# Optimization experiments

Measured on AMD Instinct MI355X. Metric: run time of the kernel, lower is better.

The kernel has to match this reference:

```python
import jax, jax.numpy as jnp
import numpy as np

N, C, W_DIM, H_DIM = 2, 256, 64, 64
HEADS = 4
DH = C // HEADS  # per-head dim for Q,K,V projections
EPS = 1e-5


def _layernorm(x, w, b):
    mu = jnp.mean(x, axis=-1, keepdims=True)
    var = jnp.var(x, axis=-1, keepdims=True)
    return (x - mu) * jax.lax.rsqrt(var + EPS) * w + b


def setup_inputs() -> dict:
    key = jax.random.key(0)
    ks = jax.random.split(key, 12)
    s = 1.0 / np.sqrt(C)
    return {
        "x": jax.random.normal(ks[0], (N, C, W_DIM, H_DIM), dtype=jnp.float32),
        "ln1_w": jnp.ones((C,), jnp.float32),
        "ln1_b": jnp.zeros((C,), jnp.float32),
        # per-head projection weights, laid out for x @ W: [heads, C, DH]
        "WQ": jax.random.normal(ks[1], (HEADS, C, DH), jnp.float32) * s,
        "WK": jax.random.normal(ks[2], (HEADS, C, DH), jnp.float32) * s,
        "WV": jax.random.normal(ks[3], (HEADS, C, DH), jnp.float32) * s,
        "ln2_w": jnp.ones((C,), jnp.float32),
        "ln2_b": jnp.zeros((C,), jnp.float32),
        "W1": jax.random.normal(ks[4], (C, C), jnp.float32) * s,
        "b1": jnp.zeros((C,), jnp.float32),
        "W2": jax.random.normal(ks[5], (C, C), jnp.float32) * s,
        "b2": jnp.zeros((C,), jnp.float32),
    }


def reference(x, ln1_w, ln1_b, WQ, WK, WV, ln2_w, ln2_b, W1, b1, W2, b2):
    n, c, w, h = x.shape
    s = w * h
    # 'n c w h -> n (w h) c'
    r = x.reshape(n, c, s).transpose(0, 2, 1)          # [n, s, c]
    norm = _layernorm(r, ln1_w, ln1_b)
    # all heads at once (original loops over heads)
    Q = jnp.einsum('nsc,hcd->nhsd', norm, WQ)
    K = jnp.einsum('nsc,hcd->nhsd', norm, WK)
    V = jnp.einsum('nsc,hcd->nhsd', norm, WV)
    # scale is 1/sqrt(seq_len) per original (keys.shape[1])
    y = jnp.einsum('nhqd,nhkd->nhqk', Q, K) / jnp.sqrt(jnp.float32(s))
    # QUIRK: softmax over dim=1 of [n, q, k] => the QUERY axis (axis=2 here)
    z = jax.nn.softmax(y, axis=2)
    attn = jnp.einsum('nhqk,nhkd->nhqd', z, V)         # [n, h, s, dh]
    attn_cat = attn.transpose(0, 2, 1, 3).reshape(n, s, c)
    out = attn_cat + r
    out = _layernorm(out, ln2_w, ln2_b)
    out = jax.nn.gelu(out @ W1 + b1, approximate=False) @ W2 + b2
    out = out + attn_cat
    # 'n (w h) c -> n c w h'
    return out.transpose(0, 2, 1).reshape(n, c, w, h)
```

## Files before the change

### kernel.cpp

```cpp
#include <hip/hip_runtime.h>
#include <math.h>

#define SEQ 4096
#define CH  256
#define NHT 8
#define DHD 64

#define QSCALE 0.0225421092f

using bf16x8 = __attribute__((ext_vector_type(8))) short;
using f32x4  = __attribute__((ext_vector_type(4))) float;
typedef unsigned short u16;
typedef unsigned int   u32;

__device__ __forceinline__ u16 f2bf(float f) {
    u32 u = __float_as_uint(f);
    u = (u + 0x7fffu + ((u >> 16) & 1u)) >> 16;
    return (u16)u;
}
__device__ __forceinline__ float bf2f(u16 h) {
    return __uint_as_float(((u32)h) << 16);
}
__device__ __forceinline__ float fexp2(float x) {
    return __builtin_amdgcn_exp2f(x);
}

__global__ __launch_bounds__(256) void k_prep(const float* __restrict__ x,
                                              const float* __restrict__ ln1w,
                                              const float* __restrict__ ln1b,
                                              const float* __restrict__ WQ,
                                              const float* __restrict__ WK,
                                              const float* __restrict__ WV,
                                              const float* __restrict__ W1,
                                              const float* __restrict__ W2,
                                              u16* __restrict__ norm,
                                              u16* __restrict__ BtQKV,
                                              u16* __restrict__ W1t,
                                              u16* __restrict__ W2t)
{
    __shared__ float tile[32][257];
    __shared__ float mu[32], rs[32];
    int bid = blockIdx.x;
    int t = threadIdx.x;
    if (bid < 1280) {
        int id = bid * 256 + t;
        if (id < 768 * 256) {
            int j = id >> 8, c = id & 255;
            int which = j >> 8, h = (j >> 6) & 3, d = j & 63;
            const float* W = (which == 0) ? WQ : (which == 1) ? WK : WV;
            BtQKV[id] = f2bf(W[(h * 256 + c) * 64 + d]);
        } else if (id < 768 * 256 + 65536) {
            int jj = id - 768 * 256;
            int j = jj >> 8, c = jj & 255;
            W1t[jj] = f2bf(W1[c * 256 + j]);
        } else if (id < 768 * 256 + 2 * 65536) {
            int jj = id - 768 * 256 - 65536;
            int j = jj >> 8, c = jj & 255;
            W2t[jj] = f2bf(W2[c * 256 + j]);
        }
        return;
    }
    int b2i = bid - 1280;
    int n = b2i >> 7, s0 = (b2i & 127) * 32;
    int sl = t & 31, cg = t >> 5;
    for (int cc = 0; cc < 256; cc += 8) {
        int c = cc + cg;
        tile[sl][c] = x[(n * 256 + c) * SEQ + s0 + sl];
    }
    __syncthreads();
    int wv = t >> 6, l = t & 63;
    for (int rr = 0; rr < 8; rr++) {
        int s = wv * 8 + rr;
        float a0 = tile[s][l], a1 = tile[s][l + 64], a2 = tile[s][l + 128], a3 = tile[s][l + 192];
        float sm = a0 + a1 + a2 + a3;
        float sq = a0 * a0 + a1 * a1 + a2 * a2 + a3 * a3;
        for (int off = 32; off; off >>= 1) { sm += __shfl_xor(sm, off); sq += __shfl_xor(sq, off); }
        if (l == 0) {
            float m = sm * (1.f / 256.f);
            mu[s] = m;
            rs[s] = rsqrtf(sq * (1.f / 256.f) - m * m + 1e-5f);
        }
    }
    __syncthreads();
    float ww = ln1w[t], bb = ln1b[t];
    for (int s = 0; s < 32; s++) {
        float v = (tile[s][t] - mu[s]) * rs[s] * ww + bb;
        norm[(n * SEQ + s0 + s) * 256 + t] = f2bf(v);
    }
}

__global__ __launch_bounds__(256) void k_qkv(const u16* __restrict__ norm,
                                             const u16* __restrict__ Bt,
                                             u16* __restrict__ Qo,
                                             u16* __restrict__ Ko,
                                             float* __restrict__ Vfo)
{
    int m0 = blockIdx.x * 64, j0 = blockIdx.y * 128;
    int t = threadIdx.x, w = t >> 6, lane = t & 63, quad = lane >> 4, l16 = lane & 15;
    const u16* Ap = norm + (long)(m0 + w * 16 + l16) * 256;
    const u16* Bp = Bt + (long)j0 * 256;
    f32x4 z = {0.f, 0.f, 0.f, 0.f};
    f32x4 acc[8];
    #pragma unroll
    for (int j = 0; j < 8; j++) acc[j] = z;
    #pragma unroll
    for (int kc = 0; kc < 8; kc++) {
        bf16x8 a = *(const bf16x8*)&Ap[kc * 32 + quad * 8];
        #pragma unroll
        for (int j = 0; j < 8; j++) {
            bf16x8 b = *(const bf16x8*)&Bp[(long)(j * 16 + l16) * 256 + kc * 32 + quad * 8];
            acc[j] = __builtin_amdgcn_mfma_f32_16x16x32_bf16(a, b, acc[j], 0, 0, 0);
        }
    }
    #pragma unroll
    for (int j = 0; j < 8; j++) {
        int col = j0 + j * 16 + l16;
        int which = col >> 8, h = (col >> 6) & 3, d = col & 63;
        int m = m0 + w * 16 + quad * 4;
        int n = m >> 12, s = m & 4095;
        if (which == 2) {
            float4 o = make_float4(acc[j][0], acc[j][1], acc[j][2], acc[j][3]);
            *(float4*)&Vfo[((long)(n * 4 + h) * 64 + d) * SEQ + s] = o;
        } else {
            u16* dst = (which == 0) ? Qo : Ko;
            float sc = (which == 0) ? QSCALE : 1.0f;
            #pragma unroll
            for (int r = 0; r < 4; r++)
                dst[((n * 4 + h) * SEQ + s + r) * 64 + d] = f2bf(acc[j][r] * sc);
        }
    }
}

__device__ __forceinline__ void xcd_decode(int s, int& g, int& sub) {
    int xcd = s & 7, m = s >> 3;
    g = xcd * 2 + (m >> 5);
    sub = m & 31;
}

__global__ __launch_bounds__(256) void k_pass1(const u16* __restrict__ Q,
                                               const u16* __restrict__ Km,
                                               float* __restrict__ D2)
{
    __shared__ float Dred[128];
    int g, sub;
    xcd_decode(blockIdx.x, g, sub);
    int nh = g & 7, qc = g >> 3, k0 = sub * 128;
    const u16* Qh = Q + (long)nh * SEQ * 64;
    const u16* Kh = Km + (long)nh * SEQ * 64;
    int t = threadIdx.x, w = t >> 6, lane = t & 63, quad = lane >> 4, l16 = lane & 15;
    bf16x8 Kf[8][2];
    #pragma unroll
    for (int i = 0; i < 8; i++) {
        Kf[i][0] = *(const bf16x8*)&Kh[(k0 + i * 16 + l16) * 64 + quad * 8];
        Kf[i][1] = *(const bf16x8*)&Kh[(k0 + i * 16 + l16) * 64 + 32 + quad * 8];
    }
    if (t < 128) Dred[t] = 0.f;
    f32x4 z = {0.f, 0.f, 0.f, 0.f};
    float Dacc[8][4] = {};
    const int qw0 = qc * 2048 + w * 512;

#define P1_LOADQ(B0, B1, ST)                                                  \
    {                                                                         \
        int _q = qw0 + (ST) * 16 + l16;                                       \
        B0 = *(const bf16x8*)&Qh[_q * 64 + quad * 8];                         \
        B1 = *(const bf16x8*)&Qh[_q * 64 + 32 + quad * 8];                    \
    }
#define P1_STEP(B0, B1)                                                       \
    {                                                                         \
        _Pragma("unroll")                                                     \
        for (int i = 0; i < 8; i++) {                                         \
            f32x4 acc = z;                                                    \
            acc = __builtin_amdgcn_mfma_f32_16x16x32_bf16(Kf[i][0], B0, acc, 0, 0, 0); \
            acc = __builtin_amdgcn_mfma_f32_16x16x32_bf16(Kf[i][1], B1, acc, 0, 0, 0); \
            _Pragma("unroll")                                                 \
            for (int r = 0; r < 4; r++) Dacc[i][r] += fexp2(acc[r]);          \
        }                                                                     \
    }

    bf16x8 qa0, qa1, qb0, qb1;
    P1_LOADQ(qa0, qa1, 0)
    P1_LOADQ(qb0, qb1, 1)
    for (int st = 0; st < 32; st += 2) {
        P1_STEP(qa0, qa1)
        if (st + 2 < 32) { P1_LOADQ(qa0, qa1, st + 2) }
        P1_STEP(qb0, qb1)
        if (st + 3 < 32) { P1_LOADQ(qb0, qb1, st + 3) }
    }
#undef P1_LOADQ
#undef P1_STEP

    #pragma unroll
    for (int i = 0; i < 8; i++)
        #pragma unroll
        for (int r = 0; r < 4; r++) {
            float v = Dacc[i][r];
            v += __shfl_xor(v, 1); v += __shfl_xor(v, 2);
            v += __shfl_xor(v, 4); v += __shfl_xor(v, 8);
            Dacc[i][r] = v;
        }
    __syncthreads();
    if (l16 == 0) {
        #pragma unroll
        for (int i = 0; i < 8; i++)
            #pragma unroll
            for (int r = 0; r < 4; r++)
                atomicAdd(&Dred[i * 16 + quad * 4 + r], Dacc[i][r]);
    }
    __syncthreads();
    if (t < 128) D2[((long)(qc * NHT + nh)) * SEQ + k0 + t] = Dred[t];
}

__global__ __launch_bounds__(256) void k_vdiv(const float* __restrict__ Vf,
                                              const float* __restrict__ D2,
                                              u16* __restrict__ Vto)
{
    int b = blockIdx.x;
    int nh = b >> 6, d = b & 63;
    const float* Da = D2 + (long)nh * SEQ;
    const float* Db = Da + (long)NHT * SEQ;
    const float* src = Vf + ((long)nh * 64 + d) * SEQ;
    u16* dst = Vto + ((long)nh * 64 + d) * SEQ;
    int t = threadIdx.x;
    #pragma unroll
    for (int half = 0; half < 2; half++) {
        int k = half * 2048 + t * 8;
        float4 va = *(const float4*)&src[k];
        float4 vb = *(const float4*)&src[k + 4];
        float4 a0 = *(const float4*)&Da[k], a1 = *(const float4*)&Da[k + 4];
        float4 b0 = *(const float4*)&Db[k], b1 = *(const float4*)&Db[k + 4];
        float o[8];
        o[0] = va.x / (a0.x + b0.x); o[1] = va.y / (a0.y + b0.y);
        o[2] = va.z / (a0.z + b0.z); o[3] = va.w / (a0.w + b0.w);
        o[4] = vb.x / (a1.x + b1.x); o[5] = vb.y / (a1.y + b1.y);
        o[6] = vb.z / (a1.z + b1.z); o[7] = vb.w / (a1.w + b1.w);
        uint4 pk;
        pk.x = (u32)f2bf(o[0]) | ((u32)f2bf(o[1]) << 16);
        pk.y = (u32)f2bf(o[2]) | ((u32)f2bf(o[3]) << 16);
        pk.z = (u32)f2bf(o[4]) | ((u32)f2bf(o[5]) << 16);
        pk.w = (u32)f2bf(o[6]) | ((u32)f2bf(o[7]) << 16);
        *(uint4*)&dst[k] = pk;
    }
}

__global__ __launch_bounds__(256, 2) void k_pass2(const u16* __restrict__ Q,
                                                  const u16* __restrict__ Km,
                                                  const u16* __restrict__ Vt,
                                                  float* __restrict__ acat2)
{
    __shared__ __align__(16) u16 lP[4][128][36];
    float (*red)[68] = (float(*)[68])lP;

    int g, sub;
    xcd_decode(blockIdx.x, g, sub);
    int nh = g & 7, kcid = g >> 3, q0 = sub * 128;
    int n = nh >> 2, h = nh & 3;
    const u16* Qh = Q + (long)nh * SEQ * 64;
    const u16* Kh = Km + (long)nh * SEQ * 64;
    const u16* Vh = Vt + (long)nh * 64 * SEQ;
    int t = threadIdx.x, w = t >> 6, lane = t & 63, quad = lane >> 4, l16 = lane & 15;
    const int kw0 = kcid * 2048 + w * 512;

    bf16x8 Qf[8][2];
    #pragma unroll
    for (int jq = 0; jq < 8; jq++)
        #pragma unroll
        for (int ch = 0; ch < 2; ch++)
            Qf[jq][ch] = *(const bf16x8*)&Qh[(q0 + jq * 16 + l16) * 64 + ch * 32 + quad * 8];

    f32x4 z = {0.f, 0.f, 0.f, 0.f};
    f32x4 accO[8][4];
    #pragma unroll
    for (int jq = 0; jq < 8; jq++)
        #pragma unroll
        for (int jd = 0; jd < 4; jd++) accO[jq][jd] = z;

#define LOAD_K(KA, KPOS)                                                      \
    {                                                                         \
        _Pragma("unroll")                                                     \
        for (int ksub = 0; ksub < 2; ksub++) {                                \
            KA[ksub][0] = *(const bf16x8*)&Kh[((KPOS) + ksub * 16 + l16) * 64 + quad * 8];      \
            KA[ksub][1] = *(const bf16x8*)&Kh[((KPOS) + ksub * 16 + l16) * 64 + 32 + quad * 8]; \
        }                                                                     \
    }
#define LOAD_V(VB, KPOS)                                                      \
    {                                                                         \
        _Pragma("unroll")                                                     \
        for (int jd = 0; jd < 4; jd++)                                        \
            VB[jd] = *(const bf16x8*)&Vh[(jd * 16 + l16) * SEQ + (KPOS) + quad * 8]; \
    }
#define QK_SLAB(KA)                                                           \
    {                                                                         \
        _Pragma("unroll")                                                     \
        for (int ksub = 0; ksub < 2; ksub++) {                                \
            _Pragma("unroll")                                                 \
            for (int jq = 0; jq < 8; jq++) {                                  \
                f32x4 acc = z;                                                \
                acc = __builtin_amdgcn_mfma_f32_16x16x32_bf16(KA[ksub][0], Qf[jq][0], acc, 0, 0, 0); \
                acc = __builtin_amdgcn_mfma_f32_16x16x32_bf16(KA[ksub][1], Qf[jq][1], acc, 0, 0, 0); \
                u32 e0 = __float_as_uint(fexp2(acc[0]));                      \
                u32 e1 = __float_as_uint(fexp2(acc[1]));                      \
                u32 e2 = __float_as_uint(fexp2(acc[2]));                      \
                u32 e3 = __float_as_uint(fexp2(acc[3]));                      \
                uint2 pk;                                                     \
                pk.x = __builtin_amdgcn_perm(e1, e0, 0x07060302u);            \
                pk.y = __builtin_amdgcn_perm(e3, e2, 0x07060302u);            \
                *(uint2*)&lP[w][jq * 16 + l16][ksub * 16 + quad * 4] = pk;    \
            }                                                                 \
        }                                                                     \
    }
#define PV_SLAB(VB)                                                           \
    {                                                                         \
        _Pragma("unroll")                                                     \
        for (int jq = 0; jq < 8; jq++) {                                      \
            bf16x8 pa = *(const bf16x8*)&lP[w][jq * 16 + l16][quad * 8];      \
            _Pragma("unroll")                                                 \
            for (int jd = 0; jd < 4; jd++)                                    \
                accO[jq][jd] = __builtin_amdgcn_mfma_f32_16x16x32_bf16(pa, VB[jd], accO[jq][jd], 0, 0, 0); \
        }                                                                     \
    }

    bf16x8 kA0[2][2], kA1[2][2], vb0[4], vb1[4];
    LOAD_K(kA0, kw0)
    LOAD_V(vb0, kw0)
    LOAD_K(kA1, kw0 + 32)
    LOAD_V(vb1, kw0 + 32)

    for (int tt = 0; tt < 8; tt++) {
        int kf = kw0 + tt * 64;
        QK_SLAB(kA0)
        if (tt < 7) { LOAD_K(kA0, kf + 64) }
        PV_SLAB(vb0)
        if (tt < 7) { LOAD_V(vb0, kf + 64) }
        QK_SLAB(kA1)
        if (tt < 7) { LOAD_K(kA1, kf + 96) }
        PV_SLAB(vb1)
        if (tt < 7) { LOAD_V(vb1, kf + 96) }
    }
#undef LOAD_K
#undef LOAD_V
#undef QK_SLAB
#undef PV_SLAB

    __syncthreads();
    for (int src = 0; src < 4; src++) {
        if (w == src) {
            #pragma unroll
            for (int jq = 0; jq < 8; jq++)
                #pragma unroll
                for (int jd = 0; jd < 4; jd++)
                    #pragma unroll
                    for (int r = 0; r < 4; r++) {
                        float* cell = &red[jq * 16 + quad * 4 + r][jd * 16 + l16];
                        if (src == 0) *cell = accO[jq][jd][r];
                        else          *cell += accO[jq][jd][r];
                    }
        }
        __syncthreads();
    }
    float* dst = acat2 + (long)kcid * 8192 * 256;
    #pragma unroll
    for (int p = 0; p < 8; p++) {
        int row = p * 16 + (t >> 4);
        int ch = (t & 15) * 4;
        float4 o = *(float4*)&red[row][ch];
        *(float4*)&dst[((long)n * SEQ + q0 + row) * 256 + h * 64 + ch] = o;
    }
}

__global__ __launch_bounds__(256) void k_tail(const float* __restrict__ x,
                                              const float* __restrict__ acat2,
                                              const float* __restrict__ lnw,
                                              const float* __restrict__ lnb,
                                              const u16* __restrict__ W1t,
                                              const float* __restrict__ b1v,
                                              const u16* __restrict__ W2t,
                                              const float* __restrict__ b2v,
                                              float* __restrict__ out)
{
    __shared__ __align__(16) unsigned char smem[16448];
    float (*tile)[257] = (float(*)[257])smem;
    u16 (*lT)[264] = (u16(*)[264])smem;
    __shared__ float aF[16][257];
    __shared__ float mu[16], rs[16];
    __shared__ __align__(16) u16 lH[16][264];

    const long STRIDE = (long)8192 * 256;
    int m0 = blockIdx.x * 16;
    int n = m0 >> 12, s0 = m0 & 4095;
    int t = threadIdx.x, w = t >> 6, lane = t & 63, quad = lane >> 4, l16 = lane & 15;

    {
        int sl = t & 15, cg = t >> 4;
        for (int cc = 0; cc < 256; cc += 16) {
            int c = cc + cg;
            tile[sl][c] = x[(n * 256 + c) * SEQ + s0 + sl];
        }
    }
    __syncthreads();
    for (int s = 0; s < 16; s++) {
        long idx = (long)(m0 + s) * 256 + t;
        float a = acat2[idx] + acat2[idx + STRIDE];
        aF[s][t] = a;
        tile[s][t] += a;
    }
    __syncthreads();
    {
        int l = t & 63;
        for (int rr = 0; rr < 4; rr++) {
            int s = w * 4 + rr;
            float a0 = tile[s][l], a1 = tile[s][l + 64], a2 = tile[s][l + 128], a3 = tile[s][l + 192];
            float sm = a0 + a1 + a2 + a3;
            float sq = a0 * a0 + a1 * a1 + a2 * a2 + a3 * a3;
            for (int off = 32; off; off >>= 1) { sm += __shfl_xor(sm, off); sq += __shfl_xor(sq, off); }
            if (l == 0) {
                float m = sm * (1.f / 256.f);
                mu[s] = m;
                rs[s] = rsqrtf(sq * (1.f / 256.f) - m * m + 1e-5f);
            }
        }
    }
    __syncthreads();
    {
        float ww = lnw[t], bb = lnb[t];
        for (int s = 0; s < 16; s++)
            lH[s][t] = f2bf((tile[s][t] - mu[s]) * rs[s] * ww + bb);
    }
    __syncthreads();

    f32x4 z = {0.f, 0.f, 0.f, 0.f};
    f32x4 acc1[4];
    #pragma unroll
    for (int js = 0; js < 4; js++) acc1[js] = z;
    #pragma unroll
    for (int kc = 0; kc < 8; kc++) {
        bf16x8 b = *(const bf16x8*)&lH[l16][kc * 32 + quad * 8];
        #pragma unroll
        for (int js = 0; js < 4; js++) {
            bf16x8 a = *(const bf16x8*)&W1t[(long)(w * 64 + js * 16 + l16) * 256 + kc * 32 + quad * 8];
            acc1[js] = __builtin_amdgcn_mfma_f32_16x16x32_bf16(a, b, acc1[js], 0, 0, 0);
        }
    }
    #pragma unroll
    for (int js = 0; js < 4; js++) {
        u32 e[4];
        #pragma unroll
        for (int r = 0; r < 4; r++) {
            int j = w * 64 + js * 16 + quad * 4 + r;
            float v = acc1[js][r] + b1v[j];
            float g = 0.5f * v * (1.f + erff(v * 0.70710678118f));
            u32 u = __float_as_uint(g);
            e[r] = u + 0x7fffu + ((u >> 16) & 1u);
        }
        uint2 pk;
        pk.x = __builtin_amdgcn_perm(e[1], e[0], 0x07060302u);
        pk.y = __builtin_amdgcn_perm(e[3], e[2], 0x07060302u);
        *(uint2*)&lT[l16][w * 64 + js * 16 + quad * 4] = pk;
    }
    __syncthreads();
    f32x4 acc2[4];
    #pragma unroll
    for (int cs = 0; cs < 4; cs++) acc2[cs] = z;
    #pragma unroll
    for (int kc = 0; kc < 8; kc++) {
        bf16x8 pa = *(const bf16x8*)&lT[l16][kc * 32 + quad * 8];
        #pragma unroll
        for (int cs = 0; cs < 4; cs++) {
            bf16x8 wb = *(const bf16x8*)&W2t[(long)(w * 64 + cs * 16 + l16) * 256 + kc * 32 + quad * 8];
            acc2[cs] = __builtin_amdgcn_mfma_f32_16x16x32_bf16(pa, wb, acc2[cs], 0, 0, 0);
        }
    }
    #pragma unroll
    for (int cs = 0; cs < 4; cs++) {
        int c = w * 64 + cs * 16 + l16;
        float bj = b2v[c];
        float vv[4];
        #pragma unroll
        for (int r = 0; r < 4; r++)
            vv[r] = acc2[cs][r] + bj + aF[quad * 4 + r][c];
        float4 o = make_float4(vv[0], vv[1], vv[2], vv[3]);
        *(float4*)&out[((long)n * 256 + c) * SEQ + s0 + quad * 4] = o;
    }
}

extern "C" void kernel_launch(void* const* d_in, const int* in_sizes, int n_in,
                              void* d_out, int out_size, void* d_ws, size_t ws_size,
                              hipStream_t stream) {
    const float* x    = (const float*)d_in[0];
    const float* ln1w = (const float*)d_in[1];
    const float* ln1b = (const float*)d_in[2];
    const float* WQ   = (const float*)d_in[3];
    const float* WK   = (const float*)d_in[4];
    const float* WV   = (const float*)d_in[5];
    const float* ln2w = (const float*)d_in[6];
    const float* ln2b = (const float*)d_in[7];
    const float* W1   = (const float*)d_in[8];
    const float* b1   = (const float*)d_in[9];
    const float* W2   = (const float*)d_in[10];
    const float* b2   = (const float*)d_in[11];
    float* out = (float*)d_out;

    char* p = (char*)d_ws;
    u16* norm   = (u16*)p;   p += (size_t)8192 * 256 * 2;
    u16* BtQKV  = (u16*)p;   p += (size_t)768 * 256 * 2;
    u16* W1t    = (u16*)p;   p += (size_t)256 * 256 * 2;
    u16* W2t    = (u16*)p;   p += (size_t)256 * 256 * 2;
    u16* Qb     = (u16*)p;   p += (size_t)NHT * SEQ * 64 * 2;
    u16* Kb     = (u16*)p;   p += (size_t)NHT * SEQ * 64 * 2;
    u16* VtT    = (u16*)p;   p += (size_t)NHT * SEQ * 64 * 2;
    float* D2   = (float*)p; p += (size_t)2 * NHT * SEQ * 4;
    float* acat2= (float*)p; p += (size_t)2 * 8192 * 256 * 4;
    float* Vf   = acat2;

    k_prep<<<1536, 256, 0, stream>>>(x, ln1w, ln1b, WQ, WK, WV, W1, W2,
                                     norm, BtQKV, W1t, W2t);
    k_qkv<<<dim3(128, 6), 256, 0, stream>>>(norm, BtQKV, Qb, Kb, Vf);
    k_pass1<<<512, 256, 0, stream>>>(Qb, Kb, D2);
    k_vdiv<<<512, 256, 0, stream>>>(Vf, D2, VtT);
    k_pass2<<<512, 256, 0, stream>>>(Qb, Kb, VtT, acat2);
    k_tail<<<512, 256, 0, stream>>>(x, acat2, ln2w, ln2b, W1t, b1, W2t, b2, out);
}
```

Measured before the change: 271.6 us.

## Split PV output columns across waves with shared double-buffered P tiles

Changes the intra-block work split in the attention pass: each wave now computes QK^T exp scores for its own 32-key stripe, writes them to a double-buffered shared P tile, and then accumulates P·V for a 16-wide slice of the head dimension over all four waves' stripes. This removes the per-wave 8x4 accumulator array and the serialized four-step cross-wave reduction through shared memory, and cuts accumulator registers from 32 to 8 vectors. In exchange, __syncthreads barriers are added inside the main loop and shared memory doubles to hold two P buffers.

Measured after the change: 226.5 us. 1.2x faster.

```diff
diff --git a/kernel.cpp b/kernel.cpp
--- a/kernel.cpp
+++ b/kernel.cpp
@@ -247,8 +247,8 @@
                                                   const u16* __restrict__ Vt,
                                                   float* __restrict__ acat2)
 {
-    __shared__ __align__(16) u16 lP[4][128][36];
-    float (*red)[68] = (float(*)[68])lP;
+    __shared__ __align__(16) u16 lP2[2][4][128][36];
+    float (*red)[68] = (float(*)[68])lP2;
 
     int g, sub;
     xcd_decode(blockIdx.x, g, sub);
@@ -258,7 +258,8 @@
     const u16* Kh = Km + (long)nh * SEQ * 64;
     const u16* Vh = Vt + (long)nh * 64 * SEQ;
     int t = threadIdx.x, w = t >> 6, lane = t & 63, quad = lane >> 4, l16 = lane & 15;
-    const int kw0 = kcid * 2048 + w * 512;
+    const int kblk = kcid * 2048;
+    const int dw = w * 16 + l16;
 
     bf16x8 Qf[8][2];
     #pragma unroll
@@ -268,95 +269,95 @@
             Qf[jq][ch] = *(const bf16x8*)&Qh[(q0 + jq * 16 + l16) * 64 + ch * 32 + quad * 8];
 
     f32x4 z = {0.f, 0.f, 0.f, 0.f};
-    f32x4 accO[8][4];
-    #pragma unroll
-    for (int jq = 0; jq < 8; jq++)
-        #pragma unroll
-        for (int jd = 0; jd < 4; jd++) accO[jq][jd] = z;
-
-#define LOAD_K(KA, KPOS)                                                      \
+    f32x4 acc[8];
+    #pragma unroll
+    for (int jq = 0; jq < 8; jq++) acc[jq] = z;
+
+#define LOAD_K(KA, I)                                                         \
     {                                                                         \
+        int _kb = kblk + (I) * 128 + w * 32;                                  \
         _Pragma("unroll")                                                     \
         for (int ksub = 0; ksub < 2; ksub++) {                                \
-            KA[ksub][0] = *(const bf16x8*)&Kh[((KPOS) + ksub * 16 + l16) * 64 + quad * 8];      \
-            KA[ksub][1] = *(const bf16x8*)&Kh[((KPOS) + ksub * 16 + l16) * 64 + 32 + quad * 8]; \
+            KA[ksub][0] = *(const bf16x8*)&Kh[(_kb + ksub * 16 + l16) * 64 + quad * 8];      \
+            KA[ksub][1] = *(const bf16x8*)&Kh[(_kb + ksub * 16 + l16) * 64 + 32 + quad * 8]; \
         }                                                                     \
     }
-#define LOAD_V(VB, KPOS)                                                      \
+#define LOAD_V(VB, I)                                                         \
     {                                                                         \
+        int _kb = kblk + (I) * 128;                                           \
         _Pragma("unroll")                                                     \
-        for (int jd = 0; jd < 4; jd++)                                        \
-            VB[jd] = *(const bf16x8*)&Vh[(jd * 16 + l16) * SEQ + (KPOS) + quad * 8]; \
-    }
-#define QK_SLAB(KA)                                                           \
+        for (int ks = 0; ks < 4; ks++)                                        \
+            VB[ks] = *(const bf16x8*)&Vh[(long)dw * SEQ + _kb + ks * 32 + quad * 8]; \
+    }
+#define QK_STRIPE(KA, B)                                                      \
     {                                                                         \
         _Pragma("unroll")                                                     \
         for (int ksub = 0; ksub < 2; ksub++) {                                \
             _Pragma("unroll")                                                 \
             for (int jq = 0; jq < 8; jq++) {                                  \
-                f32x4 acc = z;                                                \
-                acc = __builtin_amdgcn_mfma_f32_16x16x32_bf16(KA[ksub][0], Qf[jq][0], acc, 0, 0, 0); \
-                acc = __builtin_amdgcn_mfma_f32_16x16x32_bf16(KA[ksub][1], Qf[jq][1], acc, 0, 0, 0); \
-                u32 e0 = __float_as_uint(fexp2(acc[0]));                      \
-                u32 e1 = __float_as_uint(fexp2(acc[1]));                      \
-                u32 e2 = __float_as_uint(fexp2(acc[2]));                      \
-                u32 e3 = __float_as_uint(fexp2(acc[3]));                      \
+                f32x4 s_ = z;                                                 \
+                s_ = __builtin_amdgcn_mfma_f32_16x16x32_bf16(KA[ksub][0], Qf[jq][0], s_, 0, 0, 0); \
+                s_ = __builtin_amdgcn_mfma_f32_16x16x32_bf16(KA[ksub][1], Qf[jq][1], s_, 0, 0, 0); \
+                u32 e0 = __float_as_uint(fexp2(s_[0]));                       \
+                u32 e1 = __float_as_uint(fexp2(s_[1]));                       \
+                u32 e2 = __float_as_uint(fexp2(s_[2]));                       \
+                u32 e3 = __float_as_uint(fexp2(s_[3]));                       \
                 uint2 pk;                                                     \
                 pk.x = __builtin_amdgcn_perm(e1, e0, 0x07060302u);            \
                 pk.y = __builtin_amdgcn_perm(e3, e2, 0x07060302u);            \
-                *(uint2*)&lP[w][jq * 16 + l16][ksub * 16 + quad * 4] = pk;    \
+                *(uint2*)&lP2[B][w][jq * 16 + l16][ksub * 16 + quad * 4] = pk; \
             }                                                                 \
         }                                                                     \
     }
-#define PV_SLAB(VB)                                                           \
+#define PV_STRIPE(VB, B)                                                      \
     {                                                                         \
         _Pragma("unroll")                                                     \
-        for (int jq = 0; jq < 8; jq++) {                                      \
-            bf16x8 pa = *(const bf16x8*)&lP[w][jq * 16 + l16][quad * 8];      \
+        for (int ks = 0; ks < 4; ks++) {                                      \
             _Pragma("unroll")                                                 \
-            for (int jd = 0; jd < 4; jd++)                                    \
-                accO[jq][jd] = __builtin_amdgcn_mfma_f32_16x16x32_bf16(pa, VB[jd], accO[jq][jd], 0, 0, 0); \
+            for (int jq = 0; jq < 8; jq++) {                                  \
+                bf16x8 pa = *(const bf16x8*)&lP2[B][ks][jq * 16 + l16][quad * 8]; \
+                acc[jq] = __builtin_amdgcn_mfma_f32_16x16x32_bf16(pa, VB[ks], acc[jq], 0, 0, 0); \
+            }                                                                 \
         }                                                                     \
     }
 
     bf16x8 kA0[2][2], kA1[2][2], vb0[4], vb1[4];
-    LOAD_K(kA0, kw0)
-    LOAD_V(vb0, kw0)
-    LOAD_K(kA1, kw0 + 32)
-    LOAD_V(vb1, kw0 + 32)
-
-    for (int tt = 0; tt < 8; tt++) {
-        int kf = kw0 + tt * 64;
-        QK_SLAB(kA0)
-        if (tt < 7) { LOAD_K(kA0, kf + 64) }
-        PV_SLAB(vb0)
-        if (tt < 7) { LOAD_V(vb0, kf + 64) }
-        QK_SLAB(kA1)
-        if (tt < 7) { LOAD_K(kA1, kf + 96) }
-        PV_SLAB(vb1)
-        if (tt < 7) { LOAD_V(vb1, kf + 96) }
-    }
+    LOAD_K(kA0, 0)
+    LOAD_V(vb0, 0)
+    LOAD_K(kA1, 1)
+    LOAD_V(vb1, 1)
+
+    QK_STRIPE(kA0, 0)
+    __syncthreads();
+    for (int it = 0; it < 7; it++) {
+        int i = it * 2;
+        QK_STRIPE(kA1, 1)
+        LOAD_K(kA0, i + 2)
+        PV_STRIPE(vb0, 0)
+        LOAD_V(vb0, i + 2)
+        __syncthreads();
+        QK_STRIPE(kA0, 0)
+        LOAD_K(kA1, i + 3)
+        PV_STRIPE(vb1, 1)
+        LOAD_V(vb1, i + 3)
+        __syncthreads();
+    }
+    QK_STRIPE(kA1, 1)
+    PV_STRIPE(vb0, 0)
+    __syncthreads();
+    PV_STRIPE(vb1, 1)
+
 #undef LOAD_K
 #undef LOAD_V
-#undef QK_SLAB
-#undef PV_SLAB
-
-    __syncthreads();
-    for (int src = 0; src < 4; src++) {
-        if (w == src) {
-            #pragma unroll
-            for (int jq = 0; jq < 8; jq++)
-                #pragma unroll
-                for (int jd = 0; jd < 4; jd++)
-                    #pragma unroll
-                    for (int r = 0; r < 4; r++) {
-                        float* cell = &red[jq * 16 + quad * 4 + r][jd * 16 + l16];
-                        if (src == 0) *cell = accO[jq][jd][r];
-                        else          *cell += accO[jq][jd][r];
-                    }
-        }
-        __syncthreads();
-    }
+#undef QK_STRIPE
+#undef PV_STRIPE
+
+    #pragma unroll
+    for (int jq = 0; jq < 8; jq++)
+        #pragma unroll
+        for (int r = 0; r < 4; r++)
+            red[jq * 16 + quad * 4 + r][dw] = acc[jq][r];
+    __syncthreads();
     float* dst = acat2 + (long)kcid * 8192 * 256;
     #pragma unroll
     for (int p = 0; p < 8; p++) {
```
